# Kernel optimization log

Hardware: AMD Instinct MI355X
Metric: run time of the kernel (lower is better)

The kernel has to match this reference:

```python
import math
import jax, jax.numpy as jnp
import numpy as np

B, T, D_MODEL = 4, 2048, 1024
H, HD = 16, 64            # head_dim = d_model // n_heads
NF = 128                  # n_features
EPS = 1e-6
INV_SQRT_NF = 1.0 / math.sqrt(NF)


def make_orf(key, head_dim, n_features, dtype=jnp.float32):
    """Orthogonal Random Features: QR-orthogonalized gaussian blocks, scaled by sqrt(d)."""
    n_blocks = math.ceil(n_features / head_dim)
    keys = jax.random.split(key, n_blocks)
    blocks = []
    for k in keys:
        g = jax.random.normal(k, (head_dim, head_dim), dtype)
        qm, _ = jnp.linalg.qr(g)
        blocks.append(qm)
    W = jnp.concatenate(blocks, axis=1)[:, :n_features]
    return W * jnp.asarray(math.sqrt(head_dim), dtype)


def setup_inputs() -> dict:
    key = jax.random.key(0)
    k0, k1, k2, k3, k4, k5 = jax.random.split(key, 6)
    s = 1.0 / math.sqrt(D_MODEL)  # torch Linear default init scale
    x = jax.random.normal(k0, (B, T, D_MODEL), jnp.float32)
    Wq = jax.random.uniform(k1, (D_MODEL, H * HD), jnp.float32, -s, s)
    Wk = jax.random.uniform(k2, (D_MODEL, H * HD), jnp.float32, -s, s)
    Wv = jax.random.uniform(k3, (D_MODEL, H * HD), jnp.float32, -s, s)
    Wo = jax.random.uniform(k4, (H * HD, D_MODEL), jnp.float32, -s, s)
    W_feat = make_orf(k5, HD, NF)  # (HD, NF), fresh random buffer (not learned)
    return {"x": x, "Wq": Wq, "Wk": Wk, "Wv": Wv, "Wo": Wo, "W_feat": W_feat}


def _favor_plus(x, W):
    """phi(x) = exp(x.W - ||x||^2/2) / sqrt(NF); x:(B,H,T,HD) -> (B,H,T,NF)."""
    sq = 0.5 * jnp.sum(x * x, axis=-1, keepdims=True)
    return jnp.exp(x @ W - sq) * INV_SQRT_NF


def _causal_linear_attention(qp, kp, v):
    """Causal linear attention scan. qp,kp:(B,H,T,NF), v:(B,H,T,HD) -> (B,H,T,HD)."""
    Bb, Hh = qp.shape[0], qp.shape[1]

    def step(carry, qkv):
        S, z = carry  # S:(B,H,NF,HD), z:(B,H,NF)
        q_t, k_t, v_t = qkv
        S = S + jnp.einsum('bhd,bhe->bhde', k_t, v_t)
        z = z + k_t
        num = jnp.einsum('bhd,bhde->bhe', q_t, S)
        den = jnp.einsum('bhd,bhd->bh', q_t, z) + EPS
        return (S, z), num / den[..., None]

    S0 = jnp.zeros((Bb, Hh, NF, HD), qp.dtype)
    z0 = jnp.zeros((Bb, Hh, NF), qp.dtype)
    xs = (jnp.moveaxis(qp, 2, 0), jnp.moveaxis(kp, 2, 0), jnp.moveaxis(v, 2, 0))
    _, ys = jax.lax.scan(step, (S0, z0), xs)  # ys: (T,B,H,HD)
    return jnp.moveaxis(ys, 0, 2)  # (B,H,T,HD)


def reference(x, Wq, Wk, Wv, Wo, W_feat):
    Bb, Tt, _ = x.shape

    def heads(W):
        return (x @ W).reshape(Bb, Tt, H, HD).transpose(0, 2, 1, 3)  # (B,H,T,HD)

    q, k, v = heads(Wq), heads(Wk), heads(Wv)
    qp = _favor_plus(q, W_feat)
    kp = _favor_plus(k, W_feat)
    y = _causal_linear_attention(qp, kp, v)           # (B,H,T,HD)
    y = y.transpose(0, 2, 1, 3).reshape(Bb, Tt, H * HD)
    return y @ Wo
```

## Files before the change

### kernel.cpp

```cpp
#include <hip/hip_runtime.h>
#include <hip/hip_bf16.h>

typedef unsigned int u32;
typedef unsigned short u16;
typedef __bf16 bf16x8 __attribute__((ext_vector_type(8)));
typedef float f32x4 __attribute__((ext_vector_type(4)));

__device__ __forceinline__ float b2f(u16 s){ union{u32 x; float f;} c; c.x = ((u32)s) << 16; return c.f; }
__device__ __forceinline__ float b2f_lo(u32 u){ union{u32 x; float f;} c; c.x = u << 16; return c.f; }
__device__ __forceinline__ float b2f_hi(u32 u){ union{u32 x; float f;} c; c.x = u & 0xFFFF0000u; return c.f; }
__device__ __forceinline__ u16 f2b(float f){
    union{float f; u32 u;} c; c.f = f;
    u32 r = c.u + 0x7FFFu + ((c.u >> 16) & 1u);
    return (u16)(r >> 16);
}
__device__ __forceinline__ u32 pk(float lo, float hi){
    return (u32)f2b(lo) | ((u32)f2b(hi) << 16);
}
__device__ __forceinline__ void gl_lds16(const u16* g, u16* l){
    __builtin_amdgcn_global_load_lds(
        (const __attribute__((address_space(1))) void*)g,
        (__attribute__((address_space(3))) void*)l, 16, 0, 0);
}
#define BARRIER() do { __builtin_amdgcn_s_barrier(); asm volatile("" ::: "memory"); } while(0)


__global__ __launch_bounds__(256) void tobf16(const float* __restrict__ in, u16* __restrict__ out)
{
    size_t i = ((size_t)blockIdx.x * 256 + threadIdx.x) * 8;
    float4 a = *reinterpret_cast<const float4*>(in + i);
    float4 b = *reinterpret_cast<const float4*>(in + i + 4);
    uint4 v; v.x = pk(a.x, a.y); v.y = pk(a.z, a.w); v.z = pk(b.x, b.y); v.w = pk(b.z, b.w);
    *reinterpret_cast<uint4*>(out + i) = v;
}

__global__ __launch_bounds__(256) void transpose_all(const float* __restrict__ Wq, const float* __restrict__ Wk,
                                                     const float* __restrict__ Wv, const float* __restrict__ Wo,
                                                     u16* __restrict__ WTqkv, u16* __restrict__ WTo)
{
    const float* in; u16* out;
    switch (blockIdx.z){
        case 0:  in = Wq; out = WTqkv;           break;
        case 1:  in = Wk; out = WTqkv + 1048576; break;
        case 2:  in = Wv; out = WTqkv + 2097152; break;
        default: in = Wo; out = WTo;             break;
    }
    __shared__ u16 tile[64][72];
    int kb = blockIdx.x * 64, nb = blockIdx.y * 64, tid = threadIdx.x;
#pragma unroll
    for (int i = 0; i < 2; i++){
        int idx = tid + 256*i; int r = idx >> 3; int c8 = (idx & 7) * 8;
        const float* p = &in[(size_t)(kb + r)*1024 + nb + c8];
        float4 lo = *reinterpret_cast<const float4*>(p);
        float4 hi = *reinterpret_cast<const float4*>(p + 4);
        uint4 v;
        v.x = pk(lo.x, lo.y); v.y = pk(lo.z, lo.w);
        v.z = pk(hi.x, hi.y); v.w = pk(hi.z, hi.w);
        *reinterpret_cast<uint4*>(&tile[r][c8]) = v;
    }
    __syncthreads();
#pragma unroll
    for (int i = 0; i < 2; i++){
        int idx = tid + 256*i; int c = idx >> 3; int r8 = (idx & 7) * 8;
        u32 w[4];
#pragma unroll
        for (int j = 0; j < 4; j++)
            w[j] = (u32)tile[r8 + 2*j][c] | ((u32)tile[r8 + 2*j + 1][c] << 16);
        uint4 v; v.x = w[0]; v.y = w[1]; v.z = w[2]; v.w = w[3];
        *reinterpret_cast<uint4*>(&out[(size_t)(nb + c)*1024 + kb + r8]) = v;
    }
}

template<int MODE>
__global__ __launch_bounds__(512, 2) void gemm_8p(const u16* __restrict__ A, const u16* __restrict__ BT,
                                                  float* __restrict__ outf, u16* __restrict__ outh)
{
    constexpr int NT = 16;
    __shared__ u16 lds[2][24576];
    const int tid = threadIdx.x;
    const int w = tid >> 6, l = tid & 63;
    const int wr = w >> 1, wc = w & 1;
    const int fr = l & 15, q = l >> 4;
    const int m0 = blockIdx.x * 256, n0 = blockIdx.y * 128;

    const int srow = w*16 + (l >> 3);
    const int scol = ((l & 7) ^ (srow & 7)) << 3;
    const u16* Ag = A  + (size_t)(m0 + srow) * 1024 + scol;
    const u16* Bg = BT + (size_t)(n0 + srow) * 1024 + scol;
    const int sd = w*1024 + l*8;

    const int colk0 = (q*8)      ^ ((fr & 7) << 3);
    const int colk1 = (32 + q*8) ^ ((fr & 7) << 3);
    const int arow = (wr*64 + fr) * 64;
    const int brow = 16384 + (wc*64 + fr) * 64;

    f32x4 acc[4][4] = {};

#pragma unroll
    for (int kt = 0; kt < 2; ++kt){
        u16* Lb = lds[kt];
#pragma unroll
        for (int i = 0; i < 2; ++i){
            gl_lds16(Ag + (size_t)(i*8)*1024       + kt*64, Lb + sd + i*512);
            gl_lds16(Ag + (size_t)(128 + i*8)*1024 + kt*64, Lb + 8192 + sd + i*512);
            gl_lds16(Bg + (size_t)(i*8)*1024       + kt*64, Lb + 16384 + sd + i*512);
        }
    }
    asm volatile("s_waitcnt vmcnt(6)" ::: "memory");
    __builtin_amdgcn_sched_barrier(0);
    BARRIER();

    for (int t = 0; t < NT; ++t){
        u16* Lb = lds[t & 1];
        const int kt = t + 2;
        const bool st = (kt < NT);
        bf16x8 af[4][2], bfr[4][2];

#pragma unroll
        for (int i = 0; i < 4; ++i){
            af[i][0] = *reinterpret_cast<const bf16x8*>(Lb + arow + i*1024 + colk0);
            af[i][1] = *reinterpret_cast<const bf16x8*>(Lb + arow + i*1024 + colk1);
        }
#pragma unroll
        for (int j = 0; j < 4; ++j)
            bfr[j][0] = *reinterpret_cast<const bf16x8*>(Lb + brow + j*1024 + colk0);
        __builtin_amdgcn_s_barrier();
        asm volatile("s_waitcnt lgkmcnt(0)" ::: "memory");
        __builtin_amdgcn_sched_barrier(0);
        __builtin_amdgcn_s_setprio(1);
#pragma unroll
        for (int i = 0; i < 2; ++i)
#pragma unroll
            for (int j = 0; j < 4; ++j)
                acc[i][j] = __builtin_amdgcn_mfma_f32_16x16x32_bf16(af[i][0], bfr[j][0], acc[i][j], 0, 0, 0);
        __builtin_amdgcn_s_setprio(0);
        __builtin_amdgcn_sched_barrier(0);
        BARRIER();

#pragma unroll
        for (int j = 0; j < 4; ++j)
            bfr[j][1] = *reinterpret_cast<const bf16x8*>(Lb + brow + j*1024 + colk1);
        if (st){
#pragma unroll
            for (int i = 0; i < 2; ++i){
                gl_lds16(Ag + (size_t)(i*8)*1024       + kt*64, Lb + sd + i*512);
                gl_lds16(Ag + (size_t)(128 + i*8)*1024 + kt*64, Lb + 8192 + sd + i*512);
            }
        }
        __builtin_amdgcn_s_barrier();
        asm volatile("s_waitcnt lgkmcnt(0)" ::: "memory");
        __builtin_amdgcn_sched_barrier(0);
        __builtin_amdgcn_s_setprio(1);
#pragma unroll
        for (int i = 2; i < 4; ++i)
#pragma unroll
            for (int j = 0; j < 4; ++j)
                acc[i][j] = __builtin_amdgcn_mfma_f32_16x16x32_bf16(af[i][0], bfr[j][0], acc[i][j], 0, 0, 0);
        __builtin_amdgcn_s_setprio(0);
        __builtin_amdgcn_sched_barrier(0);
        BARRIER();

        if (st){
#pragma unroll
            for (int i = 0; i < 2; ++i)
                gl_lds16(Bg + (size_t)(i*8)*1024 + kt*64, Lb + 16384 + sd + i*512);
        }
        __builtin_amdgcn_s_barrier();
        __builtin_amdgcn_s_setprio(1);
#pragma unroll
        for (int i = 0; i < 2; ++i)
#pragma unroll
            for (int j = 0; j < 4; ++j)
                acc[i][j] = __builtin_amdgcn_mfma_f32_16x16x32_bf16(af[i][1], bfr[j][1], acc[i][j], 0, 0, 0);
        __builtin_amdgcn_s_setprio(0);
        __builtin_amdgcn_sched_barrier(0);
        BARRIER();

        __builtin_amdgcn_s_setprio(1);
#pragma unroll
        for (int i = 2; i < 4; ++i)
#pragma unroll
            for (int j = 0; j < 4; ++j)
                acc[i][j] = __builtin_amdgcn_mfma_f32_16x16x32_bf16(af[i][1], bfr[j][1], acc[i][j], 0, 0, 0);
        __builtin_amdgcn_s_setprio(0);
        __builtin_amdgcn_sched_barrier(0);
        if (t < NT - 2)
            asm volatile("s_waitcnt vmcnt(6)" ::: "memory");
        else
            asm volatile("s_waitcnt vmcnt(0)" ::: "memory");
        __builtin_amdgcn_sched_barrier(0);
        BARRIER();
    }

#pragma unroll
    for (int i = 0; i < 4; i++){
        int row0 = m0 + wr*64 + i*16 + q*4;
#pragma unroll
        for (int j = 0; j < 4; j++){
            int col = n0 + wc*64 + j*16 + fr;
#pragma unroll
            for (int r = 0; r < 4; r++){
                float val = acc[i][j][r];
                int row = row0 + r;
                if (MODE == 2){
                    outf[(size_t)row*1024 + col] = val;
                } else {
                    int which = col >> 10, colw = col & 1023;
                    int h = colw >> 6, d = colw & 63;
                    int bb = row >> 11, tt = row & 2047;
                    outh[(size_t)which*8388608 + (((size_t)(bb*16 + h))*2048 + tt)*64 + d] = f2b(val);
                }
            }
        }
    }
}

__global__ __launch_bounds__(256) void featmap_mfma(const u16* __restrict__ xh, const float* __restrict__ Wf,
                                                    u16* __restrict__ xp)
{
    __shared__ u16 Xl[128][72];
    __shared__ u16 Wft[128][72];
    __shared__ float sqp[128][8];
    __shared__ float sql[128];
    int tid = threadIdx.x;
    int lane = tid & 63, w = tid >> 6;
    int m = lane & 15, q = lane >> 4;
    const u16* xb = xh + (size_t)blockIdx.x * 128 * 64;
#pragma unroll
    for (int it = 0; it < 4; it++){
        int idx = tid + 256*it;
        int row = idx >> 3, c8 = (idx & 7) * 8;
        uint4 v = *reinterpret_cast<const uint4*>(xb + (size_t)row*64 + c8);
        *reinterpret_cast<uint4*>(&Xl[row][c8]) = v;
        u32 ww[4] = {v.x, v.y, v.z, v.w};
        float s = 0.f;
#pragma unroll
        for (int j = 0; j < 4; j++){
            float a = b2f_lo(ww[j]), bb = b2f_hi(ww[j]);
            s += a*a + bb*bb;
        }
        sqp[row][idx & 7] = s;
    }
#pragma unroll
    for (int it = 0; it < 8; it++){
        int idx = tid + 256*it;
        int d = idx >> 5, f4 = (idx & 31) * 4;
        float4 v = *reinterpret_cast<const float4*>(Wf + d*128 + f4);
        Wft[f4+0][d] = f2b(v.x); Wft[f4+1][d] = f2b(v.y);
        Wft[f4+2][d] = f2b(v.z); Wft[f4+3][d] = f2b(v.w);
    }
    __syncthreads();
    if (tid < 128){
        float s = 0.f;
#pragma unroll
        for (int j = 0; j < 8; j++) s += sqp[tid][j];
        sql[tid] = s;
    }
    f32x4 acc[2][8] = {};
#pragma unroll
    for (int ks = 0; ks < 2; ks++){
        bf16x8 af[2], bf[8];
#pragma unroll
        for (int mt = 0; mt < 2; mt++)
            af[mt] = *reinterpret_cast<const bf16x8*>(&Xl[32*w + mt*16 + m][ks*32 + q*8]);
#pragma unroll
        for (int nt = 0; nt < 8; nt++)
            bf[nt] = *reinterpret_cast<const bf16x8*>(&Wft[nt*16 + m][ks*32 + q*8]);
#pragma unroll
        for (int mt = 0; mt < 2; mt++)
#pragma unroll
            for (int nt = 0; nt < 8; nt++)
                acc[mt][nt] = __builtin_amdgcn_mfma_f32_16x16x32_bf16(af[mt], bf[nt], acc[mt][nt], 0, 0, 0);
    }
    __syncthreads();
    const float c = 0.08838834764831845f;
    u16* xpb = xp + (size_t)blockIdx.x * 128 * 128;
#pragma unroll
    for (int mt = 0; mt < 2; mt++){
#pragma unroll
        for (int r = 0; r < 4; r++){
            int t = 32*w + mt*16 + q*4 + r;
            float hs = 0.5f * sql[t];
#pragma unroll
            for (int nt = 0; nt < 8; nt++){
                int f = nt*16 + m;
                xpb[(size_t)t*128 + f] = f2b(__expf(fminf(acc[mt][nt][r] - hs, 60.f)) * c);
            }
        }
    }
}

struct FM1 { u16 Xl[128][72]; u16 Wft[128][72]; };
union  FMU { FM1 p1; u16 Kpt[128][136]; };
__global__ __launch_bounds__(256) void featmap_sum(const u16* __restrict__ kh, const float* __restrict__ Wf,
                                                   const u16* __restrict__ vh, u16* __restrict__ kp,
                                                   u16* __restrict__ Sa, float* __restrict__ zs)
{
    __shared__ FMU sm;
    __shared__ u16 Vt[64][136];
    __shared__ float sqp[128][8];
    __shared__ float sql[128];
    int blk = blockIdx.x, tid = threadIdx.x;
    int lane = tid & 63, w = tid >> 6;
    int m = lane & 15, q = lane >> 4;
    const u16* xb = kh + (size_t)blk * 128 * 64;
    const u16* vb = vh + (size_t)blk * 128 * 64;
#pragma unroll
    for (int it = 0; it < 4; it++){
        int idx = tid + 256*it;
        int row = idx >> 3, c8 = (idx & 7) * 8;
        uint4 v = *reinterpret_cast<const uint4*>(xb + (size_t)row*64 + c8);
        *reinterpret_cast<uint4*>(&sm.p1.Xl[row][c8]) = v;
        u32 ww[4] = {v.x, v.y, v.z, v.w};
        float s = 0.f;
#pragma unroll
        for (int j = 0; j < 4; j++){
            float a = b2f_lo(ww[j]), bb = b2f_hi(ww[j]);
            s += a*a + bb*bb;
        }
        sqp[row][idx & 7] = s;
    }
#pragma unroll
    for (int it = 0; it < 8; it++){
        int idx = tid + 256*it;
        int d = idx >> 5, f4 = (idx & 31) * 4;
        float4 v = *reinterpret_cast<const float4*>(Wf + d*128 + f4);
        sm.p1.Wft[f4+0][d] = f2b(v.x); sm.p1.Wft[f4+1][d] = f2b(v.y);
        sm.p1.Wft[f4+2][d] = f2b(v.z); sm.p1.Wft[f4+3][d] = f2b(v.w);
    }
#pragma unroll
    for (int it = 0; it < 4; it++){
        int idx = tid + 256*it;
        int t = idx >> 3, d8 = (idx & 7)*8;
        uint4 v = *reinterpret_cast<const uint4*>(vb + (size_t)t*64 + d8);
        u32 ww[4] = {v.x, v.y, v.z, v.w};
#pragma unroll
        for (int j = 0; j < 4; j++){
            Vt[d8 + 2*j][t]     = (u16)(ww[j] & 0xFFFFu);
            Vt[d8 + 2*j + 1][t] = (u16)(ww[j] >> 16);
        }
    }
    __syncthreads();
    if (tid < 128){
        float s = 0.f;
#pragma unroll
        for (int j = 0; j < 8; j++) s += sqp[tid][j];
        sql[tid] = s;
    }
    f32x4 acc[2][8] = {};
#pragma unroll
    for (int ks = 0; ks < 2; ks++){
        bf16x8 af[2], bf[8];
#pragma unroll
        for (int mt = 0; mt < 2; mt++)
            af[mt] = *reinterpret_cast<const bf16x8*>(&sm.p1.Xl[32*w + mt*16 + m][ks*32 + q*8]);
#pragma unroll
        for (int nt = 0; nt < 8; nt++)
            bf[nt] = *reinterpret_cast<const bf16x8*>(&sm.p1.Wft[nt*16 + m][ks*32 + q*8]);
#pragma unroll
        for (int mt = 0; mt < 2; mt++)
#pragma unroll
            for (int nt = 0; nt < 8; nt++)
                acc[mt][nt] = __builtin_amdgcn_mfma_f32_16x16x32_bf16(af[mt], bf[nt], acc[mt][nt], 0, 0, 0);
    }
    __syncthreads();
    const float c = 0.08838834764831845f;
    u16* xpb = kp + (size_t)blk * 128 * 128;
#pragma unroll
    for (int mt = 0; mt < 2; mt++){
#pragma unroll
        for (int r = 0; r < 4; r++){
            int t = 32*w + mt*16 + q*4 + r;
            float hs = 0.5f * sql[t];
#pragma unroll
            for (int nt = 0; nt < 8; nt++){
                int f = nt*16 + m;
                u16 pv = f2b(__expf(fminf(acc[mt][nt][r] - hs, 60.f)) * c);
                xpb[(size_t)t*128 + f] = pv;
                sm.Kpt[f][t] = pv;
            }
        }
    }
    __syncthreads();
    f32x4 acc2[8] = {};
#pragma unroll
    for (int ks = 0; ks < 4; ks++){
        bf16x8 af = *reinterpret_cast<const bf16x8*>(&Vt[16*w + m][ks*32 + q*8]);
        bf16x8 bf[8];
#pragma unroll
        for (int nt = 0; nt < 8; nt++)
            bf[nt] = *reinterpret_cast<const bf16x8*>(&sm.Kpt[nt*16 + m][ks*32 + q*8]);
#pragma unroll
        for (int nt = 0; nt < 8; nt++)
            acc2[nt] = __builtin_amdgcn_mfma_f32_16x16x32_bf16(af, bf[nt], acc2[nt], 0, 0, 0);
    }
    u16* Sb = Sa + (size_t)blk*8192;
#pragma unroll
    for (int nt = 0; nt < 8; nt++){
#pragma unroll
        for (int r = 0; r < 4; r++){
            int d = 16*w + q*4 + r;
            int f = nt*16 + m;
            Sb[(size_t)d*128 + f] = f2b(acc2[nt][r]);
        }
    }
    if (tid < 128){
        float z = 0.f;
#pragma unroll
        for (int t = 0; t < 128; t++) z += b2f(sm.Kpt[tid][t]);
        zs[(size_t)blk*128 + tid] = z;
    }
}

__global__ __launch_bounds__(256) void prefix_chunks(const u16* __restrict__ Sa, u16* __restrict__ Sb,
                                                     float* __restrict__ zs)
{
    int bh = blockIdx.x, seg = blockIdx.y, tid = threadIdx.x;
    const u16* src = Sa + (size_t)bh*16*8192;
    u16*       dst = Sb + (size_t)bh*16*8192;
#pragma unroll
    for (int it = 0; it < 4; it++){
        int e = seg*1024 + it*256 + tid;
        float run = 0.f;
#pragma unroll
        for (int c = 0; c < 16; c++){
            float v = b2f(src[(size_t)c*8192 + e]);
            dst[(size_t)c*8192 + e] = f2b(run);
            run += v;
        }
    }
    if (seg == 0 && tid < 128){
        float run = 0.f; float* zp = zs + (size_t)bh*16*128 + tid;
#pragma unroll
        for (int c = 0; c < 16; c++){ float v = zp[c*128]; zp[c*128] = run; run += v; }
    }
}

__global__ __launch_bounds__(256) void chunk_out(const u16* __restrict__ qp, const u16* __restrict__ kp,
                                                 const u16* __restrict__ vh, const u16* __restrict__ St,
                                                 const float* __restrict__ zs, u16* __restrict__ y2d)
{
    __shared__ u16 P[128][136];
    __shared__ u16 Vt[64][136];
    __shared__ u16 zl[128];
    int blk = blockIdx.x, tid = threadIdx.x;
    int lane = tid & 63, w = tid >> 6;
    int m = lane & 15, q = lane >> 4;
    int bh = blk >> 4, c = blk & 15;
    int b = bh >> 4, h = bh & 15, t0 = c*128;
    const u16* qpb = qp + ((size_t)bh*2048 + t0)*128;
    const u16* kpb = kp + ((size_t)bh*2048 + t0)*128;
    const u16* vb  = vh + ((size_t)bh*2048 + t0)*64;
    const u16* Stb = St + (size_t)blk*8192;

    if (tid < 128) zl[tid] = f2b(zs[(size_t)blk*128 + tid]);
#pragma unroll
    for (int it = 0; it < 4; it++){
        int idx = tid + 256*it;
        int t = idx >> 3, d8 = (idx & 7)*8;
        uint4 v = *reinterpret_cast<const uint4*>(&vb[(size_t)t*64 + d8]);
        u32 ww[4] = {v.x, v.y, v.z, v.w};
#pragma unroll
        for (int j = 0; j < 4; j++){
            Vt[d8 + 2*j][t]     = (u16)(ww[j] & 0xFFFFu);
            Vt[d8 + 2*j + 1][t] = (u16)(ww[j] >> 16);
        }
    }
    {
        int row = tid >> 1, half = tid & 1;
        int i = row >> 4;
        for (int s2 = 16*(i + 1) + half*2; s2 < 128; s2 += 4)
            *reinterpret_cast<u32*>(&P[row][s2]) = 0;
    }
    {
        static const unsigned char TIa[36] = {0,1,1,2,2,2,3,3,3,3,4,4,4,4,4,
                                              5,5,5,5,5,5,6,6,6,6,6,6,6,7,7,7,7,7,7,7,7};
        static const unsigned char TJa[36] = {0,0,1,0,1,2,0,1,2,3,0,1,2,3,4,
                                              0,1,2,3,4,5,0,1,2,3,4,5,6,0,1,2,3,4,5,6,7};
        for (int idx = w; idx < 36; idx += 4){
            int i = TIa[idx], j = TJa[idx];
            f32x4 a = {};
            const u16* arow = qpb + (size_t)(i*16 + m)*128 + q*8;
            const u16* brow = kpb + (size_t)(j*16 + m)*128 + q*8;
#pragma unroll
            for (int ks = 0; ks < 4; ks++){
                bf16x8 af = *reinterpret_cast<const bf16x8*>(arow + ks*32);
                bf16x8 bf = *reinterpret_cast<const bf16x8*>(brow + ks*32);
                a = __builtin_amdgcn_mfma_f32_16x16x32_bf16(af, bf, a, 0, 0, 0);
            }
            int scol = j*16 + m;
#pragma unroll
            for (int r = 0; r < 4; r++){
                int trow = i*16 + q*4 + r;
                P[trow][scol] = (scol <= trow) ? f2b(a[r]) : (u16)0;
            }
        }
    }
    __syncthreads();
    f32x4 acc[2][4] = {};
    f32x4 accd[2] = {};
    bf16x8 ones;
#pragma unroll
    for (int i = 0; i < 8; i++) ones[i] = (__bf16)1.0f;
    for (int ks = 0; ks <= w; ks++){
        bf16x8 af[2], bf4[4];
#pragma unroll
        for (int mt = 0; mt < 2; mt++)
            af[mt] = *reinterpret_cast<const bf16x8*>(&P[32*w + mt*16 + m][ks*32 + q*8]);
#pragma unroll
        for (int nt = 0; nt < 4; nt++)
            bf4[nt] = *reinterpret_cast<const bf16x8*>(&Vt[nt*16 + m][ks*32 + q*8]);
#pragma unroll
        for (int mt = 0; mt < 2; mt++){
#pragma unroll
            for (int nt = 0; nt < 4; nt++)
                acc[mt][nt] = __builtin_amdgcn_mfma_f32_16x16x32_bf16(af[mt], bf4[nt], acc[mt][nt], 0, 0, 0);
            accd[mt] = __builtin_amdgcn_mfma_f32_16x16x32_bf16(af[mt], ones, accd[mt], 0, 0, 0);
        }
    }
#pragma unroll
    for (int ks = 0; ks < 4; ks++){
        bf16x8 af[2], bf4[4];
        bf16x8 zf = *reinterpret_cast<const bf16x8*>(&zl[ks*32 + q*8]);
#pragma unroll
        for (int mt = 0; mt < 2; mt++)
            af[mt] = *reinterpret_cast<const bf16x8*>(qpb + (size_t)(32*w + mt*16 + m)*128 + ks*32 + q*8);
#pragma unroll
        for (int nt = 0; nt < 4; nt++)
            bf4[nt] = *reinterpret_cast<const bf16x8*>(Stb + (size_t)(nt*16 + m)*128 + ks*32 + q*8);
#pragma unroll
        for (int mt = 0; mt < 2; mt++){
#pragma unroll
            for (int nt = 0; nt < 4; nt++)
                acc[mt][nt] = __builtin_amdgcn_mfma_f32_16x16x32_bf16(af[mt], bf4[nt], acc[mt][nt], 0, 0, 0);
            accd[mt] = __builtin_amdgcn_mfma_f32_16x16x32_bf16(af[mt], zf, accd[mt], 0, 0, 0);
        }
    }
#pragma unroll
    for (int mt = 0; mt < 2; mt++){
#pragma unroll
        for (int nt = 0; nt < 4; nt++){
#pragma unroll
            for (int r = 0; r < 4; r++){
                int t = 32*w + mt*16 + q*4 + r;
                int d = nt*16 + m;
                float den = accd[mt][r] + 1e-6f;
                y2d[((size_t)b*2048 + t0 + t)*1024 + h*64 + d] = f2b(acc[mt][nt][r] / den);
            }
        }
    }
}

extern "C" void kernel_launch(void* const* d_in, const int* in_sizes, int n_in,
                              void* d_out, int out_size, void* d_ws, size_t ws_size,
                              hipStream_t stream)
{
    (void)in_sizes; (void)n_in; (void)out_size; (void)ws_size;
    const float* x  = (const float*)d_in[0];
    const float* Wq = (const float*)d_in[1];
    const float* Wk = (const float*)d_in[2];
    const float* Wv = (const float*)d_in[3];
    const float* Wo = (const float*)d_in[4];
    const float* Wf = (const float*)d_in[5];
    float* out = (float*)d_out;
    char* ws = (char*)d_ws;

    u16*   xh    = (u16*)  (ws + 0);
    u16*   Sa    = (u16*)  (ws + 0);
    u16*   qh    = (u16*)  (ws + 16777216);
    u16*   Sbp   = (u16*)  (ws + 16777216);
    u16*   kh    = (u16*)  (ws + 33554432);
    u16*   y2d   = (u16*)  (ws + 33554432);
    u16*   vh    = (u16*)  (ws + 50331648);
    u16*   qp    = (u16*)  (ws + 67108864);
    u16*   kp    = (u16*)  (ws + 100663296);
    u16*   WTqkv = (u16*)  (ws + 134217728);
    u16*   WTo   = (u16*)  (ws + 140509184);
    float* zs    = (float*)(ws + 142606336);

    tobf16<<<4096, 256, 0, stream>>>(x, xh);
    transpose_all<<<dim3(16, 16, 4), 256, 0, stream>>>(Wq, Wk, Wv, Wo, WTqkv, WTo);

    gemm_8p<3><<<dim3(32, 24), 512, 0, stream>>>(xh, WTqkv, nullptr, qh);

    featmap_mfma<<<1024, 256, 0, stream>>>(qh, Wf, qp);
    featmap_sum<<<1024, 256, 0, stream>>>(kh, Wf, vh, kp, Sa, zs);

    prefix_chunks<<<dim3(64, 8), 256, 0, stream>>>(Sa, Sbp, zs);
    chunk_out<<<1024, 256, 0, stream>>>(qp, kp, vh, Sbp, zs, y2d);

    gemm_8p<2><<<dim3(32, 8), 512, 0, stream>>>(y2d, WTo, out, nullptr);
}
```

Measured before the change: 296.3 us.

## Use 256x256-tile GEMM with interleaved staging for QKV projection

Adds a new gemm_256 kernel that computes 256x256 output tiles (8 waves, 128x64 per wave) with double-buffered LDS and global loads split across eight MFMA phases per k-pair. It replaces the 256x128 gemm_8p for the fused QKV projection, halving the N-direction grid and raising arithmetic intensity per loaded byte. The cost is 128 KB LDS per block and more accumulator registers, which may limit occupancy, and the grid shrinks to 384 blocks. The old gemm_8p is only tidied with macros and is still used for the output projection.

```diff
diff --git a/kernel.cpp b/kernel.cpp
--- a/kernel.cpp
+++ b/kernel.cpp
@@ -23,6 +23,19 @@
         (__attribute__((address_space(3))) void*)l, 16, 0, 0);
 }
 #define BARRIER() do { __builtin_amdgcn_s_barrier(); asm volatile("" ::: "memory"); } while(0)
+#define SCB __builtin_amdgcn_sched_barrier(0)
+#define PHASE_GATE() do { asm volatile("" ::: "memory"); __builtin_amdgcn_s_barrier(); \
+    asm volatile("s_waitcnt lgkmcnt(0)" ::: "memory"); SCB; } while(0)
+#define PHASE_END() do { SCB; __builtin_amdgcn_s_barrier(); asm volatile("" ::: "memory"); } while(0)
+#define LD8(p) (*reinterpret_cast<const bf16x8*>(p))
+#define QUAD(AF, BF, MO, NO) do { \
+    _Pragma("unroll") \
+    for (int mt = 0; mt < 4; ++mt){ \
+      _Pragma("unroll") \
+      for (int nt = 0; nt < 2; ++nt){ \
+        acc[(MO)+mt][(NO)+nt] = __builtin_amdgcn_mfma_f32_16x16x32_bf16(AF[mt][0], BF[nt][0], acc[(MO)+mt][(NO)+nt], 0,0,0); \
+        acc[(MO)+mt][(NO)+nt] = __builtin_amdgcn_mfma_f32_16x16x32_bf16(AF[mt][1], BF[nt][1], acc[(MO)+mt][(NO)+nt], 0,0,0); \
+      } } } while(0)
 
 
 __global__ __launch_bounds__(256) void tobf16(const float* __restrict__ in, u16* __restrict__ out)
@@ -72,6 +85,168 @@
 }
 
 template<int MODE>
+__global__ __launch_bounds__(512, 2) void gemm_256(const u16* __restrict__ A, const u16* __restrict__ BT,
+                                                   float* __restrict__ outf, u16* __restrict__ outh)
+{
+    __shared__ u16 lds[2][32768];
+    const int tid = threadIdx.x;
+    const int l = tid & 63, w = tid >> 6;
+    const int wr = w >> 2, wc = w & 3;
+    const int fr = l & 15, q = l >> 4;
+    const int m0 = blockIdx.x * 256, n0 = blockIdx.y * 256;
+
+    const int srow = tid >> 3;
+    const int scol = ((tid & 7) ^ (srow & 7)) << 3;
+    const u16* Ag = A  + (size_t)(m0 + srow) * 1024 + scol;
+    const u16* Bg = BT + (size_t)(n0 + srow) * 1024 + scol;
+    const int sd = tid * 8;
+
+    const int colk0 = (q*8)      ^ ((fr & 7) << 3);
+    const int colk1 = (32 + q*8) ^ ((fr & 7) << 3);
+    const int aoff = wr*8192 + fr*64;
+    const int boff = 16384 + (wc >> 1)*8192 + ((wc & 1)*64 + fr)*64;
+
+    f32x4 acc[8][4] = {};
+    bf16x8 af[4][2], bf0[2][2], bf1[2][2];
+
+    auto stgA = [&](int buf, int half, int kt){
+#pragma unroll
+        for (int i2 = 0; i2 < 2; ++i2)
+            gl_lds16(Ag + (size_t)(half*128 + i2*64)*1024 + kt*64,
+                     &lds[buf][half*8192 + i2*4096 + sd]);
+    };
+    auto stgB = [&](int buf, int half, int kt){
+#pragma unroll
+        for (int i2 = 0; i2 < 2; ++i2)
+            gl_lds16(Bg + (size_t)(half*128 + i2*64)*1024 + kt*64,
+                     &lds[buf][16384 + half*8192 + i2*4096 + sd]);
+    };
+
+    stgA(0, 0, 0); stgA(0, 1, 0); stgB(0, 0, 0); stgB(0, 1, 0);
+    stgB(1, 0, 1); stgB(1, 1, 1); stgA(1, 0, 1);
+    asm volatile("s_waitcnt vmcnt(6)" ::: "memory");
+    SCB;
+    BARRIER();
+
+    for (int i = 0; i < 8; ++i){
+        const bool s = (i < 7);
+        const int kE = 2*i + 2, kO = 2*i + 3;
+        u16* L0 = &lds[0][0];
+        u16* L1 = &lds[1][0];
+
+#pragma unroll
+        for (int mt = 0; mt < 4; ++mt){
+            af[mt][0] = LD8(L0 + aoff + mt*1024 + colk0);
+            af[mt][1] = LD8(L0 + aoff + mt*1024 + colk1);
+        }
+#pragma unroll
+        for (int nt = 0; nt < 2; ++nt){
+            bf0[nt][0] = LD8(L0 + boff + nt*1024 + colk0);
+            bf0[nt][1] = LD8(L0 + boff + nt*1024 + colk1);
+        }
+        stgA(1, 1, 2*i + 1);
+        PHASE_GATE();
+        __builtin_amdgcn_s_setprio(1); QUAD(af, bf0, 0, 0); __builtin_amdgcn_s_setprio(0);
+        PHASE_END();
+
+#pragma unroll
+        for (int nt = 0; nt < 2; ++nt){
+            bf1[nt][0] = LD8(L0 + boff + (2+nt)*1024 + colk0);
+            bf1[nt][1] = LD8(L0 + boff + (2+nt)*1024 + colk1);
+        }
+        PHASE_GATE();
+        __builtin_amdgcn_s_setprio(1); QUAD(af, bf1, 0, 2); __builtin_amdgcn_s_setprio(0);
+        PHASE_END();
+
+#pragma unroll
+        for (int mt = 0; mt < 4; ++mt){
+            af[mt][0] = LD8(L0 + aoff + 4096 + mt*1024 + colk0);
+            af[mt][1] = LD8(L0 + aoff + 4096 + mt*1024 + colk1);
+        }
+        if (s) stgB(0, 0, kE);
+        PHASE_GATE();
+        __builtin_amdgcn_s_setprio(1); QUAD(af, bf0, 4, 0); __builtin_amdgcn_s_setprio(0);
+        PHASE_END();
+
+        if (s){ stgB(0, 1, kE); stgA(0, 0, kE); }
+        PHASE_GATE();
+        __builtin_amdgcn_s_setprio(1); QUAD(af, bf1, 4, 2); __builtin_amdgcn_s_setprio(0);
+        SCB;
+        if (s) asm volatile("s_waitcnt vmcnt(6)" ::: "memory");
+        else   asm volatile("s_waitcnt vmcnt(0)" ::: "memory");
+        SCB;
+        __builtin_amdgcn_s_barrier();
+        asm volatile("" ::: "memory");
+
+#pragma unroll
+        for (int mt = 0; mt < 4; ++mt){
+            af[mt][0] = LD8(L1 + aoff + mt*1024 + colk0);
+            af[mt][1] = LD8(L1 + aoff + mt*1024 + colk1);
+        }
+#pragma unroll
+        for (int nt = 0; nt < 2; ++nt){
+            bf0[nt][0] = LD8(L1 + boff + nt*1024 + colk0);
+            bf0[nt][1] = LD8(L1 + boff + nt*1024 + colk1);
+        }
+        if (s) stgA(0, 1, kE);
+        PHASE_GATE();
+        __builtin_amdgcn_s_setprio(1); QUAD(af, bf0, 0, 0); __builtin_amdgcn_s_setprio(0);
+        PHASE_END();
+
+#pragma unroll
+        for (int nt = 0; nt < 2; ++nt){
+            bf1[nt][0] = LD8(L1 + boff + (2+nt)*1024 + colk0);
+            bf1[nt][1] = LD8(L1 + boff + (2+nt)*1024 + colk1);
+        }
+        PHASE_GATE();
+        __builtin_amdgcn_s_setprio(1); QUAD(af, bf1, 0, 2); __builtin_amdgcn_s_setprio(0);
+        PHASE_END();
+
+#pragma unroll
+        for (int mt = 0; mt < 4; ++mt){
+            af[mt][0] = LD8(L1 + aoff + 4096 + mt*1024 + colk0);
+            af[mt][1] = LD8(L1 + aoff + 4096 + mt*1024 + colk1);
+        }
+        if (s) stgB(1, 0, kO);
+        PHASE_GATE();
+        __builtin_amdgcn_s_setprio(1); QUAD(af, bf0, 4, 0); __builtin_amdgcn_s_setprio(0);
+        PHASE_END();
+
+        if (s){ stgB(1, 1, kO); stgA(1, 0, kO); }
+        PHASE_GATE();
+        __builtin_amdgcn_s_setprio(1); QUAD(af, bf1, 4, 2); __builtin_amdgcn_s_setprio(0);
+        SCB;
+        if (s) asm volatile("s_waitcnt vmcnt(6)" ::: "memory");
+        else   asm volatile("s_waitcnt vmcnt(0)" ::: "memory");
+        SCB;
+        __builtin_amdgcn_s_barrier();
+        asm volatile("" ::: "memory");
+    }
+
+#pragma unroll
+    for (int it = 0; it < 8; ++it){
+        int row0 = m0 + wr*128 + it*16 + q*4;
+#pragma unroll
+        for (int j = 0; j < 4; ++j){
+            int col = n0 + wc*64 + j*16 + fr;
+#pragma unroll
+            for (int r = 0; r < 4; ++r){
+                float val = acc[it][j][r];
+                int row = row0 + r;
+                if (MODE == 2){
+                    outf[(size_t)row*1024 + col] = val;
+                } else {
+                    int which = col >> 10, colw = col & 1023;
+                    int h = colw >> 6, d = colw & 63;
+                    int bb = row >> 11, tt = row & 2047;
+                    outh[(size_t)which*8388608 + (((size_t)(bb*16 + h))*2048 + tt)*64 + d] = f2b(val);
+                }
+            }
+        }
+    }
+}
+
+template<int MODE>
 __global__ __launch_bounds__(512, 2) void gemm_8p(const u16* __restrict__ A, const u16* __restrict__ BT,
                                                   float* __restrict__ outf, u16* __restrict__ outh)
 {
@@ -107,39 +282,36 @@
         }
     }
     asm volatile("s_waitcnt vmcnt(6)" ::: "memory");
-    __builtin_amdgcn_sched_barrier(0);
+    SCB;
     BARRIER();
 
     for (int t = 0; t < NT; ++t){
         u16* Lb = lds[t & 1];
         const int kt = t + 2;
         const bool st = (kt < NT);
-        bf16x8 af[4][2], bfr[4][2];
+        bf16x8 afv[4][2], bfr[4][2];
 
 #pragma unroll
         for (int i = 0; i < 4; ++i){
-            af[i][0] = *reinterpret_cast<const bf16x8*>(Lb + arow + i*1024 + colk0);
-            af[i][1] = *reinterpret_cast<const bf16x8*>(Lb + arow + i*1024 + colk1);
+            afv[i][0] = LD8(Lb + arow + i*1024 + colk0);
+            afv[i][1] = LD8(Lb + arow + i*1024 + colk1);
         }
 #pragma unroll
         for (int j = 0; j < 4; ++j)
-            bfr[j][0] = *reinterpret_cast<const bf16x8*>(Lb + brow + j*1024 + colk0);
-        __builtin_amdgcn_s_barrier();
-        asm volatile("s_waitcnt lgkmcnt(0)" ::: "memory");
-        __builtin_amdgcn_sched_barrier(0);
+            bfr[j][0] = LD8(Lb + brow + j*1024 + colk0);
+        PHASE_GATE();
         __builtin_amdgcn_s_setprio(1);
 #pragma unroll
         for (int i = 0; i < 2; ++i)
 #pragma unroll
             for (int j = 0; j < 4; ++j)
-                acc[i][j] = __builtin_amdgcn_mfma_f32_16x16x32_bf16(af[i][0], bfr[j][0], acc[i][j], 0, 0, 0);
+                acc[i][j] = __builtin_amdgcn_mfma_f32_16x16x32_bf16(afv[i][0], bfr[j][0], acc[i][j], 0, 0, 0);
         __builtin_amdgcn_s_setprio(0);
-        __builtin_amdgcn_sched_barrier(0);
-        BARRIER();
+        PHASE_END();
 
 #pragma unroll
         for (int j = 0; j < 4; ++j)
-            bfr[j][1] = *reinterpret_cast<const bf16x8*>(Lb + brow + j*1024 + colk1);
+            bfr[j][1] = LD8(Lb + brow + j*1024 + colk1);
         if (st){
 #pragma unroll
             for (int i = 0; i < 2; ++i){
@@ -147,18 +319,15 @@
                 gl_lds16(Ag + (size_t)(128 + i*8)*1024 + kt*64, Lb + 8192 + sd + i*512);
             }
         }
-        __builtin_amdgcn_s_barrier();
-        asm volatile("s_waitcnt lgkmcnt(0)" ::: "memory");
-        __builtin_amdgcn_sched_barrier(0);
+        PHASE_GATE();
         __builtin_amdgcn_s_setprio(1);
 #pragma unroll
         for (int i = 2; i < 4; ++i)
 #pragma unroll
             for (int j = 0; j < 4; ++j)
-                acc[i][j] = __builtin_amdgcn_mfma_f32_16x16x32_bf16(af[i][0], bfr[j][0], acc[i][j], 0, 0, 0);
+                acc[i][j] = __builtin_amdgcn_mfma_f32_16x16x32_bf16(afv[i][0], bfr[j][0], acc[i][j], 0, 0, 0);
         __builtin_amdgcn_s_setprio(0);
-        __builtin_amdgcn_sched_barrier(0);
-        BARRIER();
+        PHASE_END();
 
         if (st){
 #pragma unroll
@@ -171,24 +340,23 @@
         for (int i = 0; i < 2; ++i)
 #pragma unroll
             for (int j = 0; j < 4; ++j)
-                acc[i][j] = __builtin_amdgcn_mfma_f32_16x16x32_bf16(af[i][1], bfr[j][1], acc[i][j], 0, 0, 0);
+                acc[i][j] = __builtin_amdgcn_mfma_f32_16x16x32_bf16(afv[i][1], bfr[j][1], acc[i][j], 0, 0, 0);
         __builtin_amdgcn_s_setprio(0);
-        __builtin_amdgcn_sched_barrier(0);
-        BARRIER();
+        PHASE_END();
 
         __builtin_amdgcn_s_setprio(1);
 #pragma unroll
         for (int i = 2; i < 4; ++i)
 #pragma unroll
             for (int j = 0; j < 4; ++j)
-                acc[i][j] = __builtin_amdgcn_mfma_f32_16x16x32_bf16(af[i][1], bfr[j][1], acc[i][j], 0, 0, 0);
+                acc[i][j] = __builtin_amdgcn_mfma_f32_16x16x32_bf16(afv[i][1], bfr[j][1], acc[i][j], 0, 0, 0);
         __builtin_amdgcn_s_setprio(0);
-        __builtin_amdgcn_sched_barrier(0);
+        SCB;
         if (t < NT - 2)
             asm volatile("s_waitcnt vmcnt(6)" ::: "memory");
         else
             asm volatile("s_waitcnt vmcnt(0)" ::: "memory");
-        __builtin_amdgcn_sched_barrier(0);
+        SCB;
         BARRIER();
     }
 
@@ -581,7 +749,7 @@
     tobf16<<<4096, 256, 0, stream>>>(x, xh);
     transpose_all<<<dim3(16, 16, 4), 256, 0, stream>>>(Wq, Wk, Wv, Wo, WTqkv, WTo);
 
-    gemm_8p<3><<<dim3(32, 24), 512, 0, stream>>>(xh, WTqkv, nullptr, qh);
+    gemm_256<3><<<dim3(32, 12), 512, 0, stream>>>(xh, WTqkv, nullptr, qh);
 
     featmap_mfma<<<1024, 256, 0, stream>>>(qh, Wf, qp);
     featmap_sum<<<1024, 256, 0, stream>>>(kh, Wf, vh, kp, Sa, zs);
```

After: 296.3 us. Within noise of the previous version (+0.0%).
